# Optimization experiments

Hardware: AMD Instinct MI355X
Metric: run time of the kernel (lower is better)

Reference implementation:

```python
import jax, jax.numpy as jnp
import numpy as np
import math

B, T, C = 2, 4096, 768
NH = 12
HS = C // NH

def setup_inputs() -> dict:
    key = jax.random.key(0)
    k1, k2, k3 = jax.random.split(key, 3)
    x = jax.random.normal(k1, (B, T, C), dtype=jnp.float32)
    w_attn = jax.random.normal(k2, (C, 3 * C), dtype=jnp.float32) * (1.0 / math.sqrt(C))
    w_proj = jax.random.normal(k3, (C, C), dtype=jnp.float32) * (1.0 / math.sqrt(C))
    return {"x": x, "w_attn": w_attn, "w_proj": w_proj}

def reference(x, w_attn, w_proj):
    b, t, c = x.shape
    qkv = x @ w_attn                      # [b, t, 3c]
    q, k, v = jnp.split(qkv, 3, axis=-1)
    # [b, nh, t, hs]
    q = q.reshape(b, t, NH, HS).transpose(0, 2, 1, 3)
    k = k.reshape(b, t, NH, HS).transpose(0, 2, 1, 3)
    v = v.reshape(b, t, NH, HS).transpose(0, 2, 1, 3)
    scores = jnp.einsum('bhqd,bhkd->bhqk', q, k) / math.sqrt(HS)
    causal = jnp.tril(jnp.ones((t, t), dtype=bool))
    scores = jnp.where(causal[None, None], scores, -jnp.inf)
    att = jax.nn.softmax(scores, axis=-1)  # dropout p=0 -> identity
    out = jnp.einsum('bhqk,bhkd->bhqd', att, v)
    out = out.transpose(0, 2, 1, 3).reshape(b, t, c)
    return out @ w_proj
```

## Files before the change

### kernel.cpp

```cpp
#include <hip/hip_runtime.h>
#include <hip/hip_bf16.h>
#include <stdint.h>

#define NB 2
#define NT 4096
#define NC 768
#define NHEAD 12
#define HS 64
#define MTOK (NB * NT)
#define C3 (3 * NC)
#define CQK (2 * NC)

typedef __bf16 bf16x8 __attribute__((ext_vector_type(8)));
typedef float f32x4 __attribute__((ext_vector_type(4)));
typedef float f32x16 __attribute__((ext_vector_type(16)));

#define KSCALE_LOG2E 0.18033688011f

__device__ __forceinline__ unsigned short f2bf(float f) {
  union { float f; uint32_t u; } v; v.f = f;
  uint32_t r = v.u + 0x7fffu + ((v.u >> 16) & 1u);
  return (unsigned short)(r >> 16);
}
__device__ __forceinline__ unsigned short bft(float f) {
  return (unsigned short)(__builtin_bit_cast(unsigned int, f) >> 16);
}
__device__ __forceinline__ uint32_t pack_bf2(float a, float b) {
  return __builtin_amdgcn_perm(__builtin_bit_cast(uint32_t, a),
                               __builtin_bit_cast(uint32_t, b), 0x03020706u);
}

__device__ __forceinline__ void gload_lds16(const unsigned short* g, unsigned short* ldsbase) {
  __builtin_amdgcn_global_load_lds(
      (const __attribute__((address_space(1))) unsigned int*)g,
      (__attribute__((address_space(3))) unsigned int*)ldsbase, 16, 0, 0);
}

__device__ __forceinline__ f32x4 mfma16(bf16x8 a, bf16x8 b, f32x4 c) {
  return __builtin_amdgcn_mfma_f32_16x16x32_bf16(a, b, c, 0, 0, 0);
}
__device__ __forceinline__ f32x16 mfma32(bf16x8 a, bf16x8 b, f32x16 c) {
  return __builtin_amdgcn_mfma_f32_32x32x16_bf16(a, b, c, 0, 0, 0);
}

__global__ __launch_bounds__(256) void prep(
    const float* __restrict__ x, const float* __restrict__ wa, const float* __restrict__ wp,
    unsigned short* __restrict__ xb, unsigned short* __restrict__ waT,
    unsigned short* __restrict__ wpT) {
  const int bx = blockIdx.x;
  if (bx < 576) {
    __shared__ float tile[64][65];
    const float* src; unsigned short* dst;
    int srcN, dstN, k0, n0, qscale;
    if (bx < 432) {
      src = wa; dst = waT; srcN = C3; dstN = NC; qscale = 1;
      k0 = (bx / 36) * 64; n0 = (bx % 36) * 64;
    } else {
      const int t = bx - 432;
      src = wp; dst = wpT; srcN = NC; dstN = NC; qscale = 0;
      k0 = (t / 12) * 64; n0 = (t % 12) * 64;
    }
    const int tr = threadIdx.x >> 4;
    const int tc = (threadIdx.x & 15) * 4;
#pragma unroll
    for (int p = 0; p < 4; ++p) {
      const int r = p * 16 + tr;
      const float4 v = *reinterpret_cast<const float4*>(src + (size_t)(k0 + r) * srcN + n0 + tc);
      tile[r][tc + 0] = v.x; tile[r][tc + 1] = v.y;
      tile[r][tc + 2] = v.z; tile[r][tc + 3] = v.w;
    }
    __syncthreads();
#pragma unroll
    for (int p = 0; p < 4; ++p) {
      const int n = p * 16 + tr;
      const float sc = (qscale && (n0 + n) < NC) ? KSCALE_LOG2E : 1.0f;
      ushort4 o;
      o.x = f2bf(tile[tc + 0][n] * sc); o.y = f2bf(tile[tc + 1][n] * sc);
      o.z = f2bf(tile[tc + 2][n] * sc); o.w = f2bf(tile[tc + 3][n] * sc);
      *reinterpret_cast<ushort4*>(dst + (size_t)(n0 + n) * dstN + k0 + tc) = o;
    }
  } else {
    const int gid = (bx - 576) * 256 + threadIdx.x;
    const float4 v = reinterpret_cast<const float4*>(x)[gid];
    ushort4 o;
    o.x = f2bf(v.x); o.y = f2bf(v.y); o.z = f2bf(v.z); o.w = f2bf(v.w);
    reinterpret_cast<ushort4*>(xb)[gid] = o;
  }
}

template <int OUT_BF16>
__global__ __launch_bounds__(256) void gemm128(
    const unsigned short* __restrict__ A,
    const unsigned short* __restrict__ Bt,
    void* __restrict__ Cout,
    unsigned short* __restrict__ vT,
    int M, int N, int K, int ldc, int nx) {
  __shared__ unsigned short smem[2 * 128 * 64];
  unsigned short* As = smem;
  unsigned short* Bs = smem + 128 * 64;

  const int tid = threadIdx.x;
  const int wave = tid >> 6;
  const int lane = tid & 63;
  const int li = lane & 15;
  const int lq = lane >> 4;
  const int wm = wave & 1;
  const int wn = wave >> 1;

  const int bid = (int)blockIdx.x;
  const int nwg = (int)gridDim.x;
  const int w = (bid & 7) * (nwg >> 3) + (bid >> 3);
  const int cx = w % nx;
  const int cy = w / nx;
  const int row0 = cy * 128;
  const int col0 = cx * 128;

  const int crow = lane >> 3;
  const int cchunk = ((lane & 7) ^ crow) * 8;

  f32x4 acc[4][4] = {};

  for (int k0 = 0; k0 < K; k0 += 64) {
#pragma unroll
    for (int i = 0; i < 4; ++i) {
      const int R = wave * 32 + i * 8;
      gload_lds16(A + (size_t)(row0 + R + crow) * K + k0 + cchunk, &As[R * 64]);
      gload_lds16(Bt + (size_t)(col0 + R + crow) * K + k0 + cchunk, &Bs[R * 64]);
    }
    __syncthreads();

#pragma unroll
    for (int ks = 0; ks < 2; ++ks) {
      bf16x8 af[4], bf[4];
#pragma unroll
      for (int f = 0; f < 4; ++f) {
        const int arow = wm * 64 + f * 16 + li;
        af[f] = *reinterpret_cast<const bf16x8*>(&As[arow * 64 + (((ks * 4 + lq) ^ (li & 7)) << 3)]);
        const int brow = wn * 64 + f * 16 + li;
        bf[f] = *reinterpret_cast<const bf16x8*>(&Bs[brow * 64 + (((ks * 4 + lq) ^ (li & 7)) << 3)]);
      }
#pragma unroll
      for (int fa = 0; fa < 4; ++fa)
#pragma unroll
        for (int fb = 0; fb < 4; ++fb)
          acc[fa][fb] = mfma16(af[fa], bf[fb], acc[fa][fb]);
    }
    __syncthreads();
  }

  if (OUT_BF16) {
    if (col0 >= 2 * NC) {
      const int b = row0 >> 12;
      const int t0r = row0 & (NT - 1);
      const int h0 = (col0 - 2 * NC) >> 6;
#pragma unroll
      for (int fa = 0; fa < 4; ++fa) {
#pragma unroll
        for (int fb = 0; fb < 4; ++fb) {
          const int cc = wn * 64 + fb * 16 + li;
#pragma unroll
          for (int r = 0; r < 4; ++r) {
            const int tt = wm * 64 + fa * 16 + lq * 4 + r;
            const int slot = cc * 16 + ((tt >> 3) ^ (cc & 15));
            smem[slot * 8 + (tt & 7)] = f2bf(acc[fa][fb][r]);
          }
        }
      }
      __syncthreads();
      const int ch = tid & 15;
#pragma unroll
      for (int j = 0; j < 8; ++j) {
        const int cc = (tid >> 4) + 16 * j;
        const uint4 v = *reinterpret_cast<const uint4*>(
            smem + (size_t)(cc * 16 + (ch ^ (cc & 15))) * 8);
        const int bh = b * NHEAD + h0 + (cc >> 6);
        const int d = cc & 63;
        *reinterpret_cast<uint4*>(vT + (size_t)bh * HS * NT + (size_t)d * NT + t0r + ch * 8) = v;
      }
    } else {
      unsigned short* Cb = (unsigned short*)Cout;
#pragma unroll
      for (int fa = 0; fa < 4; ++fa) {
        const int gr = row0 + wm * 64 + fa * 16 + lq * 4;
#pragma unroll
        for (int fb = 0; fb < 4; ++fb) {
          const int gc = col0 + wn * 64 + fb * 16 + li;
#pragma unroll
          for (int r = 0; r < 4; ++r)
            Cb[(size_t)(gr + r) * ldc + gc] = f2bf(acc[fa][fb][r]);
        }
      }
    }
  } else {
    float* Cf = (float*)Cout;
#pragma unroll
    for (int fa = 0; fa < 4; ++fa) {
      const int gr = row0 + wm * 64 + fa * 16 + lq * 4;
#pragma unroll
      for (int fb = 0; fb < 4; ++fb) {
        const int gc = col0 + wn * 64 + fb * 16 + li;
#pragma unroll
        for (int r = 0; r < 4; ++r)
          Cf[(size_t)(gr + r) * ldc + gc] = acc[fa][fb][r];
      }
    }
  }
}


__global__ __launch_bounds__(256) void attn(
    const unsigned short* __restrict__ qkv,
    const unsigned short* __restrict__ vT,
    float* __restrict__ OpartA,
    float* __restrict__ OpartB,
    float* __restrict__ laccA,
    float* __restrict__ laccB) {
  __shared__ unsigned short Ks[3][64 * 64];
  __shared__ unsigned short Vts[3][64 * 64];

  const int tid = threadIdx.x;
  const int wave = tid >> 6;
  const int lane = tid & 63;
  const int l31 = lane & 31;
  const int lh = lane >> 5;
  const int sw = l31 & 7;

  const int bid = (int)blockIdx.x;
  const int xcd = bid & 7;
  const int wl = bid >> 3;
  const int grp = xcd * 3 + wl % 3;
  const int rank = wl / 3;
  const int qi = 31 - (rank >> 1);
  const int part = rank & 1;
  const int nt = 2 * qi + 2;
  const int tauS = part ? 0 : (qi + 1);
  const int tauE = part ? (qi + 1) : nt;
  const int b = grp / 12;
  const int h = grp - b * 12;
  const int q0 = qi * 128;
  const int bh = grp;

  const size_t baseQ = (size_t)b * NT * CQK + (size_t)h * HS;
  const size_t baseK = baseQ + NC;
  const unsigned short* kq = qkv + baseK;
  const unsigned short* vbase = vT + (size_t)bh * HS * NT;

  const int qw = q0 + wave * 32;
  const int qtok = qw + l31;

  bf16x8 bq[4];
#pragma unroll
  for (int ks = 0; ks < 4; ++ks)
    bq[ks] = *reinterpret_cast<const bf16x8*>(
        qkv + baseQ + (size_t)(qw + l31) * CQK + ks * 16 + lh * 8);

  bf16x8 vones;
#pragma unroll
  for (int i = 0; i < 8; ++i) vones[i] = (__bf16)1.0f;

  f32x16 o0 = {}, o1 = {}, la = {};
  const f32x16 zf = {};

  const int grow = lane >> 3;
  const int gch = (lane & 7) ^ grow;
  const int wr0 = wave * 8;
  const int wr1 = wave * 8 + 32;

#define STAGE(TAU, BUFI)                                                        \
  do {                                                                          \
    const int t0s_ = (TAU) * 64;                                                \
    gload_lds16(kq + (size_t)(t0s_ + wr0 + grow) * CQK + gch * 8,               \
                &Ks[BUFI][wr0 * 64]);                                           \
    gload_lds16(kq + (size_t)(t0s_ + wr1 + grow) * CQK + gch * 8,               \
                &Ks[BUFI][wr1 * 64]);                                           \
    gload_lds16(vbase + (size_t)(wr0 + grow) * NT + t0s_ + gch * 8,             \
                &Vts[BUFI][wr0 * 64]);                                          \
    gload_lds16(vbase + (size_t)(wr1 + grow) * NT + t0s_ + gch * 8,             \
                &Vts[BUFI][wr1 * 64]);                                          \
  } while (0)

#define EXP_PACK(ST, KBLK, DOMASK)                                             \
  do {                                                                         \
    const int kb_ = t0 + (KBLK) * 32 + 4 * lh;                                 \
    float p_[16];                                                              \
    _Pragma("unroll") for (int r = 0; r < 16; ++r) {                           \
      float v_ = (ST)[r];                                                      \
      if (DOMASK) {                                                            \
        const int kt_ = kb_ + (r & 3) + 8 * (r >> 2);                          \
        if (kt_ > qtok) v_ = -INFINITY;                                        \
      }                                                                        \
      p_[r] = __builtin_amdgcn_exp2f(v_);                                      \
    }                                                                          \
    _Pragma("unroll") for (int s = 0; s < 2; ++s) {                            \
      uint32_t a_ = pack_bf2(p_[8 * s + 0], p_[8 * s + 1]);                    \
      uint32_t b_ = pack_bf2(p_[8 * s + 2], p_[8 * s + 3]);                    \
      uint32_t c_ = pack_bf2(p_[8 * s + 4], p_[8 * s + 5]);                    \
      uint32_t d_ = pack_bf2(p_[8 * s + 6], p_[8 * s + 7]);                    \
      asm("v_permlane32_swap_b32 %0, %1" : "+v"(a_), "+v"(c_));                \
      asm("v_permlane32_swap_b32 %0, %1" : "+v"(b_), "+v"(d_));                \
      union { uint32_t u[4]; bf16x8 v8; } pu_;                                 \
      pu_.u[0] = a_; pu_.u[1] = b_; pu_.u[2] = c_; pu_.u[3] = d_;              \
      pa[2 * (KBLK) + s] = pu_.v8;                                             \
    }                                                                          \
  } while (0)

#define PV_STEP(KS)                                                            \
  do {                                                                         \
    const int off_ = ((((KS) * 2 + lh) ^ sw) << 3);                            \
    const bf16x8 bv0_ =                                                        \
        *reinterpret_cast<const bf16x8*>(Vc + (size_t)l31 * 64 + off_);        \
    const bf16x8 bv1_ =                                                        \
        *reinterpret_cast<const bf16x8*>(Vc + (size_t)(32 + l31) * 64 + off_); \
    la = mfma32(pa[KS], vones, la);                                            \
    o0 = mfma32(pa[KS], bv0_, o0);                                             \
    o1 = mfma32(pa[KS], bv1_, o1);                                             \
  } while (0)

  STAGE(tauS, 0);
  STAGE(tauS + 1, 1);

  int cur = 0;
  for (int tau = tauS; tau < tauE; ++tau) {
    const int t0 = tau * 64;
    if (tau + 1 < tauE) asm volatile("s_waitcnt vmcnt(4)" ::: "memory");
    else                asm volatile("s_waitcnt vmcnt(0)" ::: "memory");
    __builtin_amdgcn_s_barrier();
    __builtin_amdgcn_sched_barrier(0);
    if (tau + 2 < tauE) {
      int nb = cur + 2; if (nb >= 3) nb -= 3;
      STAGE(tau + 2, nb);
    }

    const unsigned short* Kc = Ks[cur];
    const unsigned short* Vc = Vts[cur];

    if (t0 <= qw + 31) {
      const bool act1 = (t0 + 32 <= qw + 31);
      const bool m0 = (t0 + 31 > qw);
      const bool m1 = (t0 + 63 > qw);

      f32x16 st0, st1;
      __builtin_amdgcn_s_setprio(1);
      {
        const bf16x8 ka0 = *reinterpret_cast<const bf16x8*>(
            Kc + (size_t)l31 * 64 + ((lh ^ sw) << 3));
        st0 = mfma32(ka0, bq[0], zf);
      }
#pragma unroll
      for (int ks = 1; ks < 4; ++ks) {
        const bf16x8 ka = *reinterpret_cast<const bf16x8*>(
            Kc + (size_t)l31 * 64 + (((ks * 2 + lh) ^ sw) << 3));
        st0 = mfma32(ka, bq[ks], st0);
      }
      if (act1) {
        {
          const bf16x8 ka0 = *reinterpret_cast<const bf16x8*>(
              Kc + (size_t)(32 + l31) * 64 + ((lh ^ sw) << 3));
          st1 = mfma32(ka0, bq[0], zf);
        }
#pragma unroll
        for (int ks = 1; ks < 4; ++ks) {
          const bf16x8 ka = *reinterpret_cast<const bf16x8*>(
              Kc + (size_t)(32 + l31) * 64 + (((ks * 2 + lh) ^ sw) << 3));
          st1 = mfma32(ka, bq[ks], st1);
        }
      }
      __builtin_amdgcn_s_setprio(0);

      bf16x8 pa[4];
      if (m0) EXP_PACK(st0, 0, 1); else EXP_PACK(st0, 0, 0);
      if (act1) {
        if (m1) EXP_PACK(st1, 1, 1); else EXP_PACK(st1, 1, 0);
      }

      __builtin_amdgcn_s_setprio(1);
      PV_STEP(0); PV_STEP(1);
      if (act1) { PV_STEP(2); PV_STEP(3); }
      __builtin_amdgcn_s_setprio(0);
    }
    ++cur; if (cur == 3) cur = 0;
  }
#undef STAGE
#undef EXP_PACK
#undef PV_STEP

  float* slotO = part ? OpartB : OpartA;
  float* lrow = (part ? laccB : laccA) + (size_t)bh * NT;
#pragma unroll
  for (int r = 0; r < 16; ++r) {
    const int q = qw + (r & 3) + 8 * (r >> 2) + 4 * lh;
    if (l31 == 0) lrow[q] = la[r];
    float* orow = slotO + ((size_t)b * NT + q) * NC + h * HS;
    orow[l31] = o0[r];
    orow[32 + l31] = o1[r];
  }
}

__global__ __launch_bounds__(256) void finalize(
    const float* __restrict__ OpartA, const float* __restrict__ OpartB,
    const float* __restrict__ laccA, const float* __restrict__ laccB,
    unsigned short* __restrict__ aob) {
  const int idx4 = (blockIdx.x * 256 + threadIdx.x);
  if (idx4 >= MTOK * NC / 4) return;
  const int idx = idx4 * 4;
  const int row = idx / NC;
  const int cc = idx - row * NC;
  const int b = row >> 12;
  const int t = row & (NT - 1);
  const int h = cc >> 6;
  const size_t lofs = (size_t)(b * NHEAD + h) * NT + t;
  const float inv = 1.0f / (laccA[lofs] + laccB[lofs]);
  const float4 v0 = *reinterpret_cast<const float4*>(OpartA + (size_t)idx);
  const float4 v1 = *reinterpret_cast<const float4*>(OpartB + (size_t)idx);
  ushort4 o;
  o.x = bft((v0.x + v1.x) * inv); o.y = bft((v0.y + v1.y) * inv);
  o.z = bft((v0.z + v1.z) * inv); o.w = bft((v0.w + v1.w) * inv);
  reinterpret_cast<ushort4*>(aob)[idx4] = o;
}

extern "C" void kernel_launch(void* const* d_in, const int* in_sizes, int n_in,
                              void* d_out, int out_size, void* d_ws, size_t ws_size,
                              hipStream_t stream) {
  const float* x = (const float*)d_in[0];
  const float* w_attn = (const float*)d_in[1];
  const float* w_proj = (const float*)d_in[2];
  float* outp = (float*)d_out;

  char* w = (char*)d_ws;
  float* OpartA = (float*)w;
  unsigned short* xb = (unsigned short*)w;
  unsigned short* waT = xb + (size_t)MTOK * NC;
  float* laccA = OpartA + (size_t)MTOK * NC;
  float* laccB = laccA + (size_t)NB * NHEAD * NT;
  unsigned short* qkvb = (unsigned short*)(laccB + (size_t)NB * NHEAD * NT);
  unsigned short* aob  = qkvb + (size_t)MTOK * CQK;
  unsigned short* vTb  = aob + (size_t)MTOK * NC;
  unsigned short* wpT  = vTb + (size_t)MTOK * NC;

  prep<<<576 + MTOK * NC / 4 / 256, 256, 0, stream>>>(x, w_attn, w_proj, xb, waT, wpT);

  gemm128<1><<<1152, 256, 0, stream>>>(
      xb, waT, qkvb, vTb, MTOK, C3, NC, CQK, C3 / 128);

  attn<<<1536, 256, 0, stream>>>(qkvb, vTb, OpartA, outp, laccA, laccB);

  finalize<<<(MTOK * NC / 4 + 255) / 256, 256, 0, stream>>>(OpartA, outp, laccA, laccB, aob);

  gemm128<0><<<384, 256, 0, stream>>>(
      aob, wpT, outp, nullptr, MTOK, NC, NC, NC, NC / 128);
}
```

Before: 219.3 us.

## Fuse split-KV finalize into attention via per-tile atomic completion counter

Removes the separate finalize kernel. Each attention block now writes its partial output, then bumps an atomic counter for its (head, query tile) pair. The second block to finish combines both partials and writes the normalized bf16 output. This saves one kernel launch and a full streaming pass over the partial buffers, at the cost of extra fences, syncthreads and a global atomic per block, with the merge load landing on whichever block finishes last. The flags are zeroed inside the prep kernel.

Measured after the change: 494.7 us. 126% more time.

```diff
diff --git a/kernel.cpp b/kernel.cpp
--- a/kernel.cpp
+++ b/kernel.cpp
@@ -46,7 +46,7 @@
 __global__ __launch_bounds__(256) void prep(
     const float* __restrict__ x, const float* __restrict__ wa, const float* __restrict__ wp,
     unsigned short* __restrict__ xb, unsigned short* __restrict__ waT,
-    unsigned short* __restrict__ wpT) {
+    unsigned short* __restrict__ wpT, unsigned int* __restrict__ flags) {
   const int bx = blockIdx.x;
   if (bx < 576) {
     __shared__ float tile[64][65];
@@ -80,6 +80,7 @@
       *reinterpret_cast<ushort4*>(dst + (size_t)(n0 + n) * dstN + k0 + tc) = o;
     }
   } else {
+    if (bx < 579) flags[(bx - 576) * 256 + threadIdx.x] = 0;
     const int gid = (bx - 576) * 256 + threadIdx.x;
     const float4 v = reinterpret_cast<const float4*>(x)[gid];
     ushort4 o;
@@ -214,9 +215,12 @@
     float* __restrict__ OpartA,
     float* __restrict__ OpartB,
     float* __restrict__ laccA,
-    float* __restrict__ laccB) {
+    float* __restrict__ laccB,
+    unsigned short* __restrict__ aob,
+    unsigned int* __restrict__ flags) {
   __shared__ unsigned short Ks[3][64 * 64];
   __shared__ unsigned short Vts[3][64 * 64];
+  __shared__ unsigned int s_old;
 
   const int tid = threadIdx.x;
   const int wave = tid >> 6;
@@ -384,38 +388,41 @@
 #undef EXP_PACK
 #undef PV_STEP
 
-  float* slotO = part ? OpartB : OpartA;
-  float* lrow = (part ? laccB : laccA) + (size_t)bh * NT;
-#pragma unroll
-  for (int r = 0; r < 16; ++r) {
-    const int q = qw + (r & 3) + 8 * (r >> 2) + 4 * lh;
-    if (l31 == 0) lrow[q] = la[r];
-    float* orow = slotO + ((size_t)b * NT + q) * NC + h * HS;
-    orow[l31] = o0[r];
-    orow[32 + l31] = o1[r];
-  }
-}
-
-__global__ __launch_bounds__(256) void finalize(
-    const float* __restrict__ OpartA, const float* __restrict__ OpartB,
-    const float* __restrict__ laccA, const float* __restrict__ laccB,
-    unsigned short* __restrict__ aob) {
-  const int idx4 = (blockIdx.x * 256 + threadIdx.x);
-  if (idx4 >= MTOK * NC / 4) return;
-  const int idx = idx4 * 4;
-  const int row = idx / NC;
-  const int cc = idx - row * NC;
-  const int b = row >> 12;
-  const int t = row & (NT - 1);
-  const int h = cc >> 6;
-  const size_t lofs = (size_t)(b * NHEAD + h) * NT + t;
-  const float inv = 1.0f / (laccA[lofs] + laccB[lofs]);
-  const float4 v0 = *reinterpret_cast<const float4*>(OpartA + (size_t)idx);
-  const float4 v1 = *reinterpret_cast<const float4*>(OpartB + (size_t)idx);
-  ushort4 o;
-  o.x = bft((v0.x + v1.x) * inv); o.y = bft((v0.y + v1.y) * inv);
-  o.z = bft((v0.z + v1.z) * inv); o.w = bft((v0.w + v1.w) * inv);
-  reinterpret_cast<ushort4*>(aob)[idx4] = o;
+  {
+    float* slotO = part ? OpartB : OpartA;
+    float* lrow = (part ? laccB : laccA) + (size_t)bh * NT;
+#pragma unroll
+    for (int r = 0; r < 16; ++r) {
+      const int q = qw + (r & 3) + 8 * (r >> 2) + 4 * lh;
+      if (l31 == 0) lrow[q] = la[r];
+      float* orow = slotO + ((size_t)b * NT + q) * NC + h * HS;
+      orow[l31] = o0[r];
+      orow[32 + l31] = o1[r];
+    }
+  }
+
+  __syncthreads();
+  __threadfence();
+  if (tid == 0) s_old = atomicAdd(&flags[bh * 32 + qi], 1u);
+  __syncthreads();
+  if (s_old == 1u) {
+    __threadfence();
+    const float* lA = laccA + (size_t)bh * NT;
+    const float* lB = laccB + (size_t)bh * NT;
+    const int c4 = (tid & 15) * 4;
+#pragma unroll
+    for (int r8 = 0; r8 < 8; ++r8) {
+      const int q = q0 + (tid >> 4) + r8 * 16;
+      const float inv = 1.0f / (lA[q] + lB[q]);
+      const size_t ofs = ((size_t)b * NT + q) * NC + h * HS + c4;
+      const float4 vA = *reinterpret_cast<const float4*>(OpartA + ofs);
+      const float4 vB = *reinterpret_cast<const float4*>(OpartB + ofs);
+      ushort4 o;
+      o.x = bft((vA.x + vB.x) * inv); o.y = bft((vA.y + vB.y) * inv);
+      o.z = bft((vA.z + vB.z) * inv); o.w = bft((vA.w + vB.w) * inv);
+      *reinterpret_cast<ushort4*>(aob + ofs) = o;
+    }
+  }
 }
 
 extern "C" void kernel_launch(void* const* d_in, const int* in_sizes, int n_in,
@@ -436,15 +443,14 @@
   unsigned short* aob  = qkvb + (size_t)MTOK * CQK;
   unsigned short* vTb  = aob + (size_t)MTOK * NC;
   unsigned short* wpT  = vTb + (size_t)MTOK * NC;
-
-  prep<<<576 + MTOK * NC / 4 / 256, 256, 0, stream>>>(x, w_attn, w_proj, xb, waT, wpT);
+  unsigned int* flags  = (unsigned int*)(wpT + (size_t)NC * NC);
+
+  prep<<<576 + MTOK * NC / 4 / 256, 256, 0, stream>>>(x, w_attn, w_proj, xb, waT, wpT, flags);
 
   gemm128<1><<<1152, 256, 0, stream>>>(
       xb, waT, qkvb, vTb, MTOK, C3, NC, CQK, C3 / 128);
 
-  attn<<<1536, 256, 0, stream>>>(qkvb, vTb, OpartA, outp, laccA, laccB);
-
-  finalize<<<(MTOK * NC / 4 + 255) / 256, 256, 0, stream>>>(OpartA, outp, laccA, laccB, aob);
+  attn<<<1536, 256, 0, stream>>>(qkvb, vTb, OpartA, outp, laccA, laccB, aob, flags);
 
   gemm128<0><<<384, 256, 0, stream>>>(
       aob, wpT, outp, nullptr, MTOK, NC, NC, NC, NC / 128);
```
